# Kernel optimization log

Measured on AMD Instinct MI355X. Metric: run time of the kernel, lower is better.

The kernel has to match this reference:

```python
import jax, jax.numpy as jnp
import numpy as np

H = 16
D_MODEL = 1024
B, S = 4, 2048
D_K = D_MODEL // H


def setup_inputs() -> dict:
    key = jax.random.key(0)
    ks = jax.random.split(key, 12)
    sc = 1.0 / np.sqrt(D_MODEL)
    inp = {
        "query": jax.random.normal(ks[0], (B, S, D_MODEL), jnp.float32),
        "key": jax.random.normal(ks[1], (B, S, D_MODEL), jnp.float32),
        "value": jax.random.normal(ks[2], (B, S, D_MODEL), jnp.float32),
        "mask": jnp.ones((B, 1, S, S), dtype=bool),
        "Wq": jax.random.normal(ks[3], (D_MODEL, D_MODEL), jnp.float32) * sc,
        "bq": jnp.zeros((D_MODEL,), jnp.float32),
        "Wk": jax.random.normal(ks[4], (D_MODEL, D_MODEL), jnp.float32) * sc,
        "bk": jnp.zeros((D_MODEL,), jnp.float32),
        "Wv": jax.random.normal(ks[5], (D_MODEL, D_MODEL), jnp.float32) * sc,
        "bv": jnp.zeros((D_MODEL,), jnp.float32),
        "Wo": jax.random.normal(ks[6], (D_MODEL, D_MODEL), jnp.float32) * sc,
        "bo": jnp.zeros((D_MODEL,), jnp.float32),
    }
    return inp


def reference(query, key, value, mask, Wq, bq, Wk, bk, Wv, bv, Wo, bo):
    b, s, d = query.shape

    def proj(x, W, bias):
        # nn.Linear: x @ W.T + b, then split heads -> [b, h, s, d_k]
        return (x @ W.T + bias).reshape(b, -1, H, D_K).transpose(0, 2, 1, 3)

    q = proj(query, Wq, bq)
    k = proj(key, Wk, bk)
    v = proj(value, Wv, bv)

    scores = jnp.einsum("bhqd,bhkd->bhqk", q, k) / np.sqrt(D_K).astype(np.float32)
    scores = jnp.where(mask, scores, jnp.float32(-1e9))  # masked_fill(mask==0, -inf)
    attn = jax.nn.softmax(scores, axis=-1)  # dropout = identity in eval
    x = jnp.einsum("bhqk,bhkd->bhqd", attn, v)
    x = x.transpose(0, 2, 1, 3).reshape(b, -1, H * D_K)
    return x @ Wo.T + bo
```

## Files before the change

kernel.cpp:

```cpp
#include <hip/hip_runtime.h>
#include <hip/hip_bf16.h>
#include <stdint.h>

#define B_   4
#define S_   2048
#define H_   16
#define DK_  64
#define D_   1024

typedef unsigned short u16;
typedef unsigned int   u32;
typedef __bf16 bf16x8  __attribute__((ext_vector_type(8)));
typedef __bf16 bf16x2_t __attribute__((ext_vector_type(2)));
typedef float  floatx4 __attribute__((ext_vector_type(4)));
typedef float  floatx16 __attribute__((ext_vector_type(16)));
typedef u32    u32x2   __attribute__((ext_vector_type(2)));
typedef u32    u32x4   __attribute__((ext_vector_type(4)));

__device__ __forceinline__ u16 f2bf(float x) {
    u32 u = __builtin_bit_cast(u32, x);
    return (u16)((u + 0x7FFFu + ((u >> 16) & 1u)) >> 16);
}

__device__ __forceinline__ u32 pk2bf(float a, float b) {
    bf16x2_t r; r[0] = (__bf16)a; r[1] = (__bf16)b;
    return __builtin_bit_cast(u32, r);
}

struct u32pair { u32 x, y; };
#if __has_builtin(__builtin_amdgcn_permlane32_swap)
__device__ __forceinline__ u32pair lane32swap(u32 a, u32 b) {
    u32x2 r = __builtin_amdgcn_permlane32_swap(a, b, false, false);
    return { r[0], r[1] };
}
#else
__device__ __forceinline__ u32pair lane32swap(u32 a, u32 b) {
    u32 bs = __shfl_xor((unsigned int)b, 32, 64);
    u32 as = __shfl_xor((unsigned int)a, 32, 64);
    bool lo = ((threadIdx.x & 63) < 32);
    u32pair r; r.x = lo ? a : bs; r.y = lo ? as : b; return r;
}
#endif

#if __has_builtin(__builtin_amdgcn_exp2f)
#define EXP2F(x) __builtin_amdgcn_exp2f(x)
#else
#define EXP2F(x) exp2f(x)
#endif

__device__ __forceinline__ void glds16(const void* g, void* l) {
    __builtin_amdgcn_global_load_lds((const __attribute__((address_space(1))) void*)g,
                                     (__attribute__((address_space(3))) void*)l, 16, 0, 0);
}

__global__ __launch_bounds__(256)
void k_cvt7(const float* __restrict__ x0, const float* __restrict__ x1, const float* __restrict__ x2,
            const float* __restrict__ w0, const float* __restrict__ w1,
            const float* __restrict__ w2, const float* __restrict__ w3,
            u16* __restrict__ y0, u16* __restrict__ y1, u16* __restrict__ y2,
            u16* __restrict__ v0, u16* __restrict__ v1, u16* __restrict__ v2, u16* __restrict__ v3)
{
    int i = blockIdx.x;
    const float* s; u16* d; size_t off;
    if (i < 12288) {
        int z = i >> 12;
        s = (z == 0) ? x0 : (z == 1) ? x1 : x2;
        d = (z == 0) ? y0 : (z == 1) ? y1 : y2;
        off = (size_t)(i & 4095) * 2048;
    } else {
        int j = i - 12288;
        int z = j >> 9;
        s = (z == 0) ? w0 : (z == 1) ? w1 : (z == 2) ? w2 : w3;
        d = (z == 0) ? v0 : (z == 1) ? v1 : (z == 2) ? v2 : v3;
        off = (size_t)(j & 511) * 2048;
    }
    size_t idx = off + (size_t)threadIdx.x * 8;
    float4 a = *(const float4*)(s + idx);
    float4 b = *(const float4*)(s + idx + 4);
    u32x4 o;
    o[0] = pk2bf(a.x, a.y);
    o[1] = pk2bf(a.z, a.w);
    o[2] = pk2bf(b.x, b.y);
    o[3] = pk2bf(b.z, b.w);
    *(u32x4*)(d + idx) = o;
}

__device__ __forceinline__ void gemm_core(const u16* __restrict__ A, const u16* __restrict__ Bm,
                                          int m0, int n0, floatx4 (&acc)[4][4],
                                          u16* As, u16* Bs)
{
    const int tid = threadIdx.x, lane = tid & 63, w = tid >> 6;
    const int wm = (w & 1) * 64, wn = (w >> 1) * 64;
    const int lr = lane & 15, quad = lane >> 4;
    const int srow = lane >> 3, sj0 = lane & 7;
    const int j = sj0 ^ srow;

#pragma unroll
    for (int t = 0; t < 4; t++) {
        int blk = w * 4 + t;
        int row = blk * 8 + srow;
        glds16(A  + (size_t)(m0 + row) * 1024 + j * 8, &As[blk * 512]);
        glds16(Bm + (size_t)(n0 + row) * 1024 + j * 8, &Bs[blk * 512]);
    }
    __syncthreads();

    for (int k0 = 0; k0 < 1024; k0 += 64) {
        bf16x8 af0[4], bf0[4], af1[4], bf1[4];
#pragma unroll
        for (int mt = 0; mt < 4; mt++) {
            int row = wm + mt * 16 + lr;
            af0[mt] = *(const bf16x8*)&As[row * 64 + ((quad ^ (row & 7)) * 8)];
        }
#pragma unroll
        for (int nt = 0; nt < 4; nt++) {
            int row = wn + nt * 16 + lr;
            bf0[nt] = *(const bf16x8*)&Bs[row * 64 + ((quad ^ (row & 7)) * 8)];
        }
#pragma unroll
        for (int mt = 0; mt < 4; mt++)
#pragma unroll
            for (int nt = 0; nt < 4; nt++)
                acc[mt][nt] = __builtin_amdgcn_mfma_f32_16x16x32_bf16(af0[mt], bf0[nt], acc[mt][nt], 0, 0, 0);
#pragma unroll
        for (int mt = 0; mt < 4; mt++) {
            int row = wm + mt * 16 + lr;
            af1[mt] = *(const bf16x8*)&As[row * 64 + (((4 + quad) ^ (row & 7)) * 8)];
        }
#pragma unroll
        for (int nt = 0; nt < 4; nt++) {
            int row = wn + nt * 16 + lr;
            bf1[nt] = *(const bf16x8*)&Bs[row * 64 + (((4 + quad) ^ (row & 7)) * 8)];
        }
        __syncthreads();
        if (k0 + 64 < 1024) {
#pragma unroll
            for (int t = 0; t < 4; t++) {
                int blk = w * 4 + t;
                int row = blk * 8 + srow;
                glds16(A  + (size_t)(m0 + row) * 1024 + (k0 + 64) + j * 8, &As[blk * 512]);
                glds16(Bm + (size_t)(n0 + row) * 1024 + (k0 + 64) + j * 8, &Bs[blk * 512]);
            }
        }
#pragma unroll
        for (int mt = 0; mt < 4; mt++)
#pragma unroll
            for (int nt = 0; nt < 4; nt++)
                acc[mt][nt] = __builtin_amdgcn_mfma_f32_16x16x32_bf16(af1[mt], bf1[nt], acc[mt][nt], 0, 0, 0);
        __syncthreads();
    }
}

__device__ __forceinline__ void epi_heads(floatx4 (&acc)[4][4], const float* bias,
                                          u16* O, int m0, int n0, float scale)
{
    const int tid = threadIdx.x, lane = tid & 63, w = tid >> 6;
    const int wm = (w & 1) * 64, wn = (w >> 1) * 64;
    const int lr = lane & 15, quad = lane >> 4;
#pragma unroll
    for (int nt = 0; nt < 4; nt++) {
        int n = n0 + wn + nt * 16 + lr; float bb = bias[n];
        int h = n >> 6, dk = n & 63;
#pragma unroll
        for (int mt = 0; mt < 4; mt++)
#pragma unroll
            for (int r = 0; r < 4; r++) {
                int m = m0 + wm + mt * 16 + quad * 4 + r;
                int b = m >> 11, s = m & 2047;
                O[(size_t)((b * 16 + h) * 2048 + s) * 64 + dk] = f2bf((acc[mt][nt][r] + bb) * scale);
            }
    }
}

__global__ __launch_bounds__(512, 2)
void k_qkv256(const u16* __restrict__ Xqb, const u16* __restrict__ Xkb, const u16* __restrict__ Xvb,
              const u16* __restrict__ Wb,
              const float* __restrict__ bq, const float* __restrict__ bk, const float* __restrict__ bv,
              u16* __restrict__ Qg, u16* __restrict__ Kg, u16* __restrict__ Vt, float qscale)
{
    __shared__ __align__(16) u16 As[2][256 * 64];
    __shared__ __align__(16) u16 Bs[2][256 * 64];

    const int m0  = blockIdx.x * 256;
    const int ny  = blockIdx.y;
    const int z   = ny >> 2;
    const int nl0 = (ny & 3) * 256;

    const u16* A = (z == 0) ? Xqb : (z == 1) ? Xkb : Xvb;
    const u16* W = Wb + (u32)z * 1048576u;
    const float* bias = (z == 0) ? bq : (z == 1) ? bk : bv;

    const int tid = threadIdx.x, lane = tid & 63, w = tid >> 6;
    const int wm = (w & 1) * 128, wn = (w >> 1) * 64;
    const int lr = lane & 15, quad = lane >> 4;
    const int srow = lane >> 3, sj0 = lane & 7;
    const int gcol = (sj0 ^ srow) * 8;

    floatx4 acc[8][4];
#pragma unroll
    for (int mi = 0; mi < 8; mi++)
#pragma unroll
        for (int ni = 0; ni < 4; ni++) acc[mi][ni] = (floatx4)0.0f;

#pragma unroll
    for (int t8 = 0; t8 < 4; t8++) {
        int bi = w * 4 + t8;
        int row = bi * 8 + srow;
        glds16(A + (size_t)(m0 + row) * 1024 + gcol, &As[0][bi * 512]);
        glds16(W + (size_t)(nl0 + row) * 1024 + gcol, &Bs[0][bi * 512]);
    }
    __syncthreads();

    for (int t = 0; t < 16; t++) {
        const int p = t & 1;
        const u16* Ab = As[p];
        const u16* Bb = Bs[p];
        bf16x8 bf[4];
#pragma unroll
        for (int ph = 0; ph < 4; ph++) {
            const int h = ph >> 1, mg = ph & 1;
            if (mg == 0) {
#pragma unroll
                for (int ni = 0; ni < 4; ni++) {
                    int row = wn + ni * 16 + lr;
                    bf[ni] = *(const bf16x8*)&Bb[row * 64 + (((h * 4 + quad) ^ (row & 7)) * 8)];
                }
            }
            bf16x8 af[4];
#pragma unroll
            for (int j = 0; j < 4; j++) {
                int row = wm + (mg * 4 + j) * 16 + lr;
                af[j] = *(const bf16x8*)&Ab[row * 64 + (((h * 4 + quad) ^ (row & 7)) * 8)];
            }
            if (ph < 2 && t + 1 < 16) {
                const int kk = (t + 1) * 64;
#pragma unroll
                for (int t8 = ph * 2; t8 < ph * 2 + 2; t8++) {
                    int bi = w * 4 + t8;
                    int row = bi * 8 + srow;
                    glds16(A + (size_t)(m0 + row) * 1024 + kk + gcol, &As[p ^ 1][bi * 512]);
                    glds16(W + (size_t)(nl0 + row) * 1024 + kk + gcol, &Bs[p ^ 1][bi * 512]);
                }
            }
            __builtin_amdgcn_s_setprio(1);
#pragma unroll
            for (int j = 0; j < 4; j++)
#pragma unroll
                for (int ni = 0; ni < 4; ni++)
                    acc[mg * 4 + j][ni] = __builtin_amdgcn_mfma_f32_16x16x32_bf16(af[j], bf[ni], acc[mg * 4 + j][ni], 0, 0, 0);
            __builtin_amdgcn_s_setprio(0);
        }
        __syncthreads();
    }

    const float scl = (z == 0) ? qscale : 1.0f;
#pragma unroll
    for (int ni = 0; ni < 4; ni++) {
        int n = nl0 + wn + ni * 16 + lr;
        float bb = bias[n];
        if (z == 2) {
#pragma unroll
            for (int mi = 0; mi < 8; mi++)
#pragma unroll
                for (int r = 0; r < 4; r++) {
                    int m = m0 + wm + mi * 16 + quad * 4 + r;
                    Vt[(size_t)n * 8192 + m] = f2bf(acc[mi][ni][r] + bb);
                }
        } else {
            u16* O = (z == 0) ? Qg : Kg;
            int hh = n >> 6, dk = n & 63;
#pragma unroll
            for (int mi = 0; mi < 8; mi++)
#pragma unroll
                for (int r = 0; r < 4; r++) {
                    int m = m0 + wm + mi * 16 + quad * 4 + r;
                    int b = m >> 11, s = m & 2047;
                    O[(size_t)((b * 16 + hh) * 2048 + s) * 64 + dk] = f2bf((acc[mi][ni][r] + bb) * scl);
                }
        }
    }
}

__global__ __launch_bounds__(256, 3)
void k_gemm(const u16* __restrict__ A, const u16* __restrict__ Bm,
            const float* __restrict__ bias, void* __restrict__ outp,
            int mode, float scale)
{
    const int m0 = (mode == 2) ? blockIdx.y * 128 : blockIdx.x * 128;
    const int n0 = (mode == 2) ? blockIdx.x * 128 : blockIdx.y * 128;
    __shared__ __align__(16) u16 As[128 * 64];
    __shared__ __align__(16) u16 Bs[128 * 64];

    floatx4 acc[4][4];
#pragma unroll
    for (int i = 0; i < 4; i++)
#pragma unroll
        for (int j = 0; j < 4; j++) acc[i][j] = (floatx4)0.0f;

    gemm_core(A, Bm, m0, n0, acc, As, Bs);

    const int tid = threadIdx.x, lane = tid & 63, w = tid >> 6;
    const int wm = (w & 1) * 64, wn = (w >> 1) * 64;
    const int lr = lane & 15, quad = lane >> 4;

    if (mode == 3) {
        float* O = (float*)outp;
#pragma unroll
        for (int nt = 0; nt < 4; nt++) {
            int n = n0 + wn + nt * 16 + lr; float bb = bias[n];
#pragma unroll
            for (int mt = 0; mt < 4; mt++)
#pragma unroll
                for (int r = 0; r < 4; r++) {
                    int m = m0 + wm + mt * 16 + quad * 4 + r;
                    O[(size_t)m * 1024 + n] = acc[mt][nt][r] + bb;
                }
        }
    } else if (mode == 2) {
        u16* O = (u16*)outp;
#pragma unroll
        for (int mt = 0; mt < 4; mt++)
#pragma unroll
            for (int r = 0; r < 4; r++) {
                int f = m0 + wm + mt * 16 + quad * 4 + r; float bm = bias[f];
#pragma unroll
                for (int nt = 0; nt < 4; nt++) {
                    int n = n0 + wn + nt * 16 + lr;
                    O[(size_t)f * 8192 + n] = f2bf(acc[mt][nt][r] + bm);
                }
            }
    } else {
        epi_heads(acc, bias, (u16*)outp, m0, n0, scale);
    }
}

__global__ __launch_bounds__(256, 2)
void k_attn(const u16* __restrict__ Qg, const u16* __restrict__ Kg,
            const u16* __restrict__ Vt, u16* __restrict__ Xa)
{
    const int bh = blockIdx.x, bb = bh >> 4, h = bh & 15;
    const int q0 = blockIdx.y * 256;
    const int tid = threadIdx.x, lane = tid & 63, w = tid >> 6;
    const int lm = lane & 31, half = lane >> 5;
    const int srow = lane >> 3, sj0 = lane & 7;

    __shared__ __align__(16) u16 Ks[2][64 * 64];
    __shared__ __align__(16) u16 Vs[2][64 * 64];

#pragma unroll
    for (int t = 0; t < 2; t++) {
        int blk = w * 2 + t;
        int row = blk * 8 + srow;
        glds16(Kg + ((size_t)bh * 2048 + row) * 64 + (sj0 ^ srow) * 8, &Ks[0][blk * 512]);
        glds16(Vt + ((size_t)(h * 64 + row)) * 8192 + bb * 2048 + (sj0 ^ srow) * 8, &Vs[0][blk * 512]);
    }

    bf16x8 qf[2][4];
#pragma unroll
    for (int qs = 0; qs < 2; qs++) {
        const u16* qbase = Qg + ((size_t)bh * 2048 + q0 + w * 64 + qs * 32 + lm) * 64;
#pragma unroll
        for (int ks = 0; ks < 4; ks++)
            qf[qs][ks] = *(const bf16x8*)(qbase + (ks * 2 + half) * 8);
    }

    floatx16 acc_o[2][2], acc_l[2];
#pragma unroll
    for (int qs = 0; qs < 2; qs++) {
        acc_l[qs] = (floatx16)0.0f;
#pragma unroll
        for (int vt = 0; vt < 2; vt++) acc_o[qs][vt] = (floatx16)0.0f;
    }
    u32x4 ow; ow[0] = 0x3F803F80u; ow[1] = 0x3F803F80u; ow[2] = 0x3F803F80u; ow[3] = 0x3F803F80u;
    const bf16x8 ones = __builtin_bit_cast(bf16x8, ow);

    __syncthreads();

    for (int kt = 0; kt < 32; kt++) {
        const int p = kt & 1;

        bf16x8 af[2][4], bv[2][4];
#pragma unroll
        for (int ks = 0; ks < 4; ks++)
#pragma unroll
            for (int mt = 0; mt < 2; mt++) {
                int row = mt * 32 + lm;
                int ch  = (ks * 2 + half) ^ (lm & 7);
                af[mt][ks] = *(const bf16x8*)&Ks[p][row * 64 + ch * 8];
                bv[mt][ks] = *(const bf16x8*)&Vs[p][row * 64 + ch * 8];
            }

        if (kt + 1 < 32) {
            const int kb2 = (kt + 1) * 64;
#pragma unroll
            for (int t = 0; t < 2; t++) {
                int blk = w * 2 + t;
                int row = blk * 8 + srow;
                glds16(Kg + ((size_t)bh * 2048 + kb2 + row) * 64 + (sj0 ^ srow) * 8, &Ks[p ^ 1][blk * 512]);
                glds16(Vt + ((size_t)(h * 64 + row)) * 8192 + bb * 2048 + kb2 + (sj0 ^ srow) * 8, &Vs[p ^ 1][blk * 512]);
            }
        }

        floatx16 sa[2][2];
#pragma unroll
        for (int mt = 0; mt < 2; mt++)
#pragma unroll
            for (int qs = 0; qs < 2; qs++) sa[mt][qs] = (floatx16)0.0f;
#pragma unroll
        for (int ks = 0; ks < 4; ks++)
#pragma unroll
            for (int mt = 0; mt < 2; mt++)
#pragma unroll
                for (int qs = 0; qs < 2; qs++)
                    sa[mt][qs] = __builtin_amdgcn_mfma_f32_32x32x16_bf16(af[mt][ks], qf[qs][ks], sa[mt][qs], 0, 0, 0);

#pragma unroll
        for (int mt = 0; mt < 2; mt++) {
            bf16x8 pm[2][2];
#pragma unroll
            for (int qs = 0; qs < 2; qs++) {
                float e[16];
#pragma unroll
                for (int i = 0; i < 16; i++) e[i] = EXP2F(sa[mt][qs][i]);
                u32 p0[4], p1[4];
#pragma unroll
                for (int g = 0; g < 4; g++) {
                    p0[g] = pk2bf(e[4 * g], e[4 * g + 1]);
                    p1[g] = pk2bf(e[4 * g + 2], e[4 * g + 3]);
                }
#pragma unroll
                for (int g2 = 0; g2 < 2; g2++) {
                    u32pair r0 = lane32swap(p0[2 * g2], p0[2 * g2 + 1]);
                    u32pair r1 = lane32swap(p1[2 * g2], p1[2 * g2 + 1]);
                    u32x4 t4; t4[0] = r0.x; t4[1] = r1.x; t4[2] = r0.y; t4[3] = r1.y;
                    pm[qs][g2] = __builtin_bit_cast(bf16x8, t4);
                }
            }
#pragma unroll
            for (int g2 = 0; g2 < 2; g2++) {
                int s = mt * 2 + g2;
#pragma unroll
                for (int qs = 0; qs < 2; qs++) {
                    acc_l[qs] = __builtin_amdgcn_mfma_f32_32x32x16_bf16(pm[qs][g2], ones, acc_l[qs], 0, 0, 0);
#pragma unroll
                    for (int vt = 0; vt < 2; vt++)
                        acc_o[qs][vt] = __builtin_amdgcn_mfma_f32_32x32x16_bf16(pm[qs][g2], bv[vt][s], acc_o[qs][vt], 0, 0, 0);
                }
            }
        }

        __syncthreads();
    }

#pragma unroll
    for (int qs = 0; qs < 2; qs++) {
        float inv[16];
#pragma unroll
        for (int i = 0; i < 16; i++) inv[i] = 1.0f / acc_l[qs][i];
#pragma unroll
        for (int vt = 0; vt < 2; vt++)
#pragma unroll
            for (int i = 0; i < 16; i++) {
                int row = (i & 3) + 8 * (i >> 2) + 4 * half;
                int q   = q0 + w * 64 + qs * 32 + row;
                int dk  = vt * 32 + lm;
                Xa[((size_t)(bb * 2048 + q)) * 1024 + h * 64 + dk] = f2bf(acc_o[qs][vt][i] * inv[i]);
            }
    }
}

extern "C" void kernel_launch(void* const* d_in, const int* in_sizes, int n_in,
                              void* d_out, int out_size, void* d_ws, size_t ws_size,
                              hipStream_t stream)
{
    const float* Xq = (const float*)d_in[0];
    const float* Xk = (const float*)d_in[1];
    const float* Xv = (const float*)d_in[2];
    const float* Wq = (const float*)d_in[4];
    const float* bq = (const float*)d_in[5];
    const float* Wk = (const float*)d_in[6];
    const float* bk = (const float*)d_in[7];
    const float* Wv = (const float*)d_in[8];
    const float* bv = (const float*)d_in[9];
    const float* Wo = (const float*)d_in[10];
    const float* bo = (const float*)d_in[11];
    float* Out = (float*)d_out;

    const float QSCALE = 0.18033688f;
    const size_t T = 8388608u;

    u16* Wb = (u16*)d_ws;

    if (ws_size >= (4u * 1048576u + 6u * T) * sizeof(u16)) {
        u16* Xqb = Wb + 4u * 1048576u;
        u16* Xkb = Xqb + T;
        u16* Xvb = Xkb + T;
        u16* Qg  = Xvb + T;
        u16* Kg  = Qg + T;
        u16* Vt  = Kg + T;
        u16* Xa  = Xqb;

        k_cvt7<<<dim3(14336), 256, 0, stream>>>(Xq, Xk, Xv, Wq, Wk, Wv, Wo,
                                                Xqb, Xkb, Xvb,
                                                Wb, Wb + 1048576u, Wb + 2097152u, Wb + 3145728u);
        k_qkv256<<<dim3(32, 12), 512, 0, stream>>>(Xqb, Xkb, Xvb, Wb, bq, bk, bv,
                                                   Qg, Kg, Vt, QSCALE);
        k_attn<<<dim3(64, 8), 256, 0, stream>>>(Qg, Kg, Vt, Xa);
        k_gemm<<<dim3(64, 8), 256, 0, stream>>>(Xa, Wb + 3145728u, bo, Out, 3, 1.0f);
    } else {
        u16* slot0 = Wb + 4u * 1048576u;
        u16* slot1 = slot0 + T;
        u16* slot2 = slot1 + T;
        u16* slot3 = slot2 + T;

        k_cvt7<<<dim3(14336), 256, 0, stream>>>(Xq, Xk, Xv, Wq, Wk, Wv, Wo,
                                                slot0, slot1, slot2,
                                                Wb, Wb + 1048576u, Wb + 2097152u, Wb + 3145728u);
        k_gemm<<<dim3(64, 8), 256, 0, stream>>>(slot0, Wb, bq, slot3, 0, QSCALE);
        k_gemm<<<dim3(64, 8), 256, 0, stream>>>(slot1, Wb + 1048576u, bk, slot0, 1, 1.0f);
        k_gemm<<<dim3(64, 8), 256, 0, stream>>>(Wb + 2097152u, slot2, bv, slot1, 2, 1.0f);
        k_attn<<<dim3(64, 8), 256, 0, stream>>>(slot3, slot0, slot1, slot2);
        k_gemm<<<dim3(64, 8), 256, 0, stream>>>(slot2, Wb + 3145728u, bo, Out, 3, 1.0f);
    }
}
```

Baseline: 360.9 us.

## Rewrite QKV projection GEMM with 4-slot K=32 pipeline and swapped V operands

Measured after the change: 376.2 us. +4.2%, slower.

```diff
diff --git a/kernel.cpp b/kernel.cpp
--- a/kernel.cpp
+++ b/kernel.cpp
@@ -172,28 +172,27 @@
 }
 
 __global__ __launch_bounds__(512, 2)
-void k_qkv256(const u16* __restrict__ Xqb, const u16* __restrict__ Xkb, const u16* __restrict__ Xvb,
-              const u16* __restrict__ Wb,
-              const float* __restrict__ bq, const float* __restrict__ bk, const float* __restrict__ bv,
-              u16* __restrict__ Qg, u16* __restrict__ Kg, u16* __restrict__ Vt, float qscale)
-{
-    __shared__ __align__(16) u16 As[2][256 * 64];
-    __shared__ __align__(16) u16 Bs[2][256 * 64];
-
-    const int m0  = blockIdx.x * 256;
-    const int ny  = blockIdx.y;
-    const int z   = ny >> 2;
-    const int nl0 = (ny & 3) * 256;
-
-    const u16* A = (z == 0) ? Xqb : (z == 1) ? Xkb : Xvb;
-    const u16* W = Wb + (u32)z * 1048576u;
-    const float* bias = (z == 0) ? bq : (z == 1) ? bk : bv;
+void k_qkvp(const u16* __restrict__ Xqb, const u16* __restrict__ Xkb, const u16* __restrict__ Xvb,
+            const u16* __restrict__ Wb,
+            const float* __restrict__ bq, const float* __restrict__ bk, const float* __restrict__ bv,
+            u16* __restrict__ Qg, u16* __restrict__ Kg, u16* __restrict__ Vt, float qscale)
+{
+    __shared__ __align__(16) u16 AsR[4 * 256 * 32];
+    __shared__ __align__(16) u16 BsR[4 * 256 * 32];
+
+    const int bx = blockIdx.x, ny = blockIdx.y;
+    const int z = ny >> 2, nq = ny & 3;
+
+    const u16 *Ap, *Bp;
+    int m0, n0;
+    if (z == 2) { Ap = Wb + 2u * 1048576u; Bp = Xvb; m0 = nq * 256; n0 = bx * 256; }
+    else        { Ap = (z == 0) ? Xqb : Xkb; Bp = Wb + (u32)z * 1048576u; m0 = bx * 256; n0 = nq * 256; }
 
     const int tid = threadIdx.x, lane = tid & 63, w = tid >> 6;
     const int wm = (w & 1) * 128, wn = (w >> 1) * 64;
     const int lr = lane & 15, quad = lane >> 4;
-    const int srow = lane >> 3, sj0 = lane & 7;
-    const int gcol = (sj0 ^ srow) * 8;
+    const int rsub = lane >> 2;
+    const int cg   = (lane & 3) ^ (rsub & 3);
 
     floatx4 acc[8][4];
 #pragma unroll
@@ -201,72 +200,75 @@
 #pragma unroll
         for (int ni = 0; ni < 4; ni++) acc[mi][ni] = (floatx4)0.0f;
 
-#pragma unroll
-    for (int t8 = 0; t8 < 4; t8++) {
-        int bi = w * 4 + t8;
-        int row = bi * 8 + srow;
-        glds16(A + (size_t)(m0 + row) * 1024 + gcol, &As[0][bi * 512]);
-        glds16(W + (size_t)(nl0 + row) * 1024 + gcol, &Bs[0][bi * 512]);
-    }
-    __syncthreads();
-
-    for (int t = 0; t < 16; t++) {
-        const int p = t & 1;
-        const u16* Ab = As[p];
-        const u16* Bb = Bs[p];
-        bf16x8 bf[4];
-#pragma unroll
-        for (int ph = 0; ph < 4; ph++) {
-            const int h = ph >> 1, mg = ph & 1;
-            if (mg == 0) {
-#pragma unroll
-                for (int ni = 0; ni < 4; ni++) {
-                    int row = wn + ni * 16 + lr;
-                    bf[ni] = *(const bf16x8*)&Bb[row * 64 + (((h * 4 + quad) ^ (row & 7)) * 8)];
-                }
-            }
-            bf16x8 af[4];
-#pragma unroll
-            for (int j = 0; j < 4; j++) {
-                int row = wm + (mg * 4 + j) * 16 + lr;
-                af[j] = *(const bf16x8*)&Ab[row * 64 + (((h * 4 + quad) ^ (row & 7)) * 8)];
-            }
-            if (ph < 2 && t + 1 < 16) {
-                const int kk = (t + 1) * 64;
-#pragma unroll
-                for (int t8 = ph * 2; t8 < ph * 2 + 2; t8++) {
-                    int bi = w * 4 + t8;
-                    int row = bi * 8 + srow;
-                    glds16(A + (size_t)(m0 + row) * 1024 + kk + gcol, &As[p ^ 1][bi * 512]);
-                    glds16(W + (size_t)(nl0 + row) * 1024 + kk + gcol, &Bs[p ^ 1][bi * 512]);
-                }
-            }
-            __builtin_amdgcn_s_setprio(1);
-#pragma unroll
-            for (int j = 0; j < 4; j++)
-#pragma unroll
-                for (int ni = 0; ni < 4; ni++)
-                    acc[mg * 4 + j][ni] = __builtin_amdgcn_mfma_f32_16x16x32_bf16(af[j], bf[ni], acc[mg * 4 + j][ni], 0, 0, 0);
-            __builtin_amdgcn_s_setprio(0);
-        }
-        __syncthreads();
-    }
-
-    const float scl = (z == 0) ? qscale : 1.0f;
-#pragma unroll
-    for (int ni = 0; ni < 4; ni++) {
-        int n = nl0 + wn + ni * 16 + lr;
-        float bb = bias[n];
-        if (z == 2) {
+    auto STAGE = [&](int jj) {
+        const int slot = jj & 3;
+        const int kb   = jj * 32;
+        u16* sA = AsR + slot * 8192;
+        u16* sB = BsR + slot * 8192;
+#pragma unroll
+        for (int s = 0; s < 2; s++) {
+            int rowb = w * 32 + s * 16;
+            int row  = rowb + rsub;
+            glds16(Ap + (size_t)(m0 + row) * 1024 + kb + cg * 8, sA + rowb * 32);
+            glds16(Bp + (size_t)(n0 + row) * 1024 + kb + cg * 8, sB + rowb * 32);
+        }
+    };
+
+    STAGE(0); STAGE(1); STAGE(2);
+    asm volatile("s_waitcnt vmcnt(8)" ::: "memory");
+    __builtin_amdgcn_s_barrier();
+    __builtin_amdgcn_sched_barrier(0);
+
+    for (int j = 0; j < 32; ++j) {
+        if (j + 3 < 32) STAGE(j + 3);
+
+        const u16* sA = AsR + (j & 3) * 8192;
+        const u16* sB = BsR + (j & 3) * 8192;
+        bf16x8 af[8], bf[4];
+#pragma unroll
+        for (int mi = 0; mi < 8; mi++) {
+            int row = wm + mi * 16 + lr;
+            af[mi] = *(const bf16x8*)&sA[row * 32 + ((quad ^ (row & 3)) * 8)];
+        }
+#pragma unroll
+        for (int ni = 0; ni < 4; ni++) {
+            int row = wn + ni * 16 + lr;
+            bf[ni] = *(const bf16x8*)&sB[row * 32 + ((quad ^ (row & 3)) * 8)];
+        }
+
+        __builtin_amdgcn_s_setprio(1);
+#pragma unroll
+        for (int mi = 0; mi < 8; mi++)
+#pragma unroll
+            for (int ni = 0; ni < 4; ni++)
+                acc[mi][ni] = __builtin_amdgcn_mfma_f32_16x16x32_bf16(af[mi], bf[ni], acc[mi][ni], 0, 0, 0);
+        __builtin_amdgcn_s_setprio(0);
+
+        if (j < 29) asm volatile("s_waitcnt vmcnt(8)" ::: "memory");
+        else        asm volatile("s_waitcnt vmcnt(0)" ::: "memory");
+        __builtin_amdgcn_s_barrier();
+        __builtin_amdgcn_sched_barrier(0);
+    }
+
+    if (z == 2) {
+#pragma unroll
+        for (int ni = 0; ni < 4; ni++) {
+            int tok = n0 + wn + ni * 16 + lr;
 #pragma unroll
             for (int mi = 0; mi < 8; mi++)
 #pragma unroll
                 for (int r = 0; r < 4; r++) {
-                    int m = m0 + wm + mi * 16 + quad * 4 + r;
-                    Vt[(size_t)n * 8192 + m] = f2bf(acc[mi][ni][r] + bb);
-                }
-        } else {
-            u16* O = (z == 0) ? Qg : Kg;
+                    int f = m0 + wm + mi * 16 + quad * 4 + r;
+                    Vt[(size_t)f * 8192 + tok] = f2bf(acc[mi][ni][r] + bv[f]);
+                }
+        }
+    } else {
+        const float* bias = (z == 0) ? bq : bk;
+        u16* O = (z == 0) ? Qg : Kg;
+        const float scl = (z == 0) ? qscale : 1.0f;
+#pragma unroll
+        for (int ni = 0; ni < 4; ni++) {
+            int n = n0 + wn + ni * 16 + lr; float bb = bias[n];
             int hh = n >> 6, dk = n & 63;
 #pragma unroll
             for (int mi = 0; mi < 8; mi++)
@@ -502,8 +504,8 @@
         k_cvt7<<<dim3(14336), 256, 0, stream>>>(Xq, Xk, Xv, Wq, Wk, Wv, Wo,
                                                 Xqb, Xkb, Xvb,
                                                 Wb, Wb + 1048576u, Wb + 2097152u, Wb + 3145728u);
-        k_qkv256<<<dim3(32, 12), 512, 0, stream>>>(Xqb, Xkb, Xvb, Wb, bq, bk, bv,
-                                                   Qg, Kg, Vt, QSCALE);
+        k_qkvp<<<dim3(32, 12), 512, 0, stream>>>(Xqb, Xkb, Xvb, Wb, bq, bk, bv,
+                                                 Qg, Kg, Vt, QSCALE);
         k_attn<<<dim3(64, 8), 256, 0, stream>>>(Qg, Kg, Vt, Xa);
         k_gemm<<<dim3(64, 8), 256, 0, stream>>>(Xa, Wb + 3145728u, bo, Out, 3, 1.0f);
     } else {
```
